# Performance work log

Hardware: AMD Instinct MI355X
Metric: run time of the kernel (lower is better)

The kernel has to match this reference:

```python
import jax, jax.numpy as jnp
import numpy as np

NUM_REL = 5000
NUM_BIN = 32
NUM_EDGES = 200000
DIM = 512
NUM_HEAD = 8
DIM_HID = DIM // NUM_HEAD


def setup_inputs() -> dict:
    key = jax.random.key(0)
    ks = jax.random.split(key, 10)
    emb_rel = jax.random.normal(ks[0], (NUM_REL, DIM), dtype=jnp.float32)
    emb_bin = jax.random.normal(ks[1], (NUM_BIN, DIM), dtype=jnp.float32)
    head = jax.random.randint(ks[2], (NUM_EDGES, 1), 0, NUM_REL)
    tail = jax.random.randint(ks[3], (NUM_EDGES, 1), 0, NUM_REL)
    bins = jax.random.randint(ks[4], (NUM_EDGES, 1), 0, NUM_BIN)
    relation_triplets = jnp.concatenate([head, tail, bins], axis=1).astype(jnp.int64)
    gain = float(np.sqrt(2.0))  # calculate_gain('relu')
    # xavier normal: std = gain * sqrt(2/(fan_in+fan_out))
    std_attn = gain * np.sqrt(2.0 / (3 * DIM + DIM))
    std_aggr = gain * np.sqrt(2.0 / (DIM + DIM))
    std_vec = gain * np.sqrt(2.0 / (NUM_HEAD + DIM_HID))
    W_attn = std_attn * jax.random.normal(ks[5], (DIM, 3 * DIM), dtype=jnp.float32)
    b_attn = jnp.zeros((DIM,), dtype=jnp.float32)
    attn_vec = std_vec * jax.random.normal(ks[6], (1, NUM_HEAD, DIM_HID), dtype=jnp.float32)
    W_aggr = std_aggr * jax.random.normal(ks[7], (DIM, DIM), dtype=jnp.float32)
    b_aggr = jnp.zeros((DIM,), dtype=jnp.float32)
    return {"emb_rel": emb_rel, "emb_bin": emb_bin, "relation_triplets": relation_triplets,
            "W_attn": W_attn, "b_attn": b_attn, "attn_vec": attn_vec,
            "W_aggr": W_aggr, "b_aggr": b_aggr}


def reference(emb_rel, emb_bin, relation_triplets, W_attn, b_attn, attn_vec, W_aggr, b_aggr):
    num_rel = emb_rel.shape[0]
    head = relation_triplets[:, 0]
    tail = relation_triplets[:, 1]
    bins = relation_triplets[:, 2]
    # gather + concat -> [E, 3*D]
    concat = jnp.concatenate([emb_rel[head], emb_bin[bins], emb_rel[tail]], axis=-1)
    h = jax.nn.leaky_relu(concat @ W_attn.T + b_attn, negative_slope=0.2)
    h = h.reshape(-1, NUM_HEAD, DIM_HID)
    attn_raw = jnp.sum(h * attn_vec, axis=-1)  # [E, H]
    # segmented softmax over edges sharing the same head relation
    seg_max = jax.ops.segment_max(attn_raw, head, num_segments=num_rel)  # [R, H]
    seg_max = jnp.where(jnp.isfinite(seg_max), seg_max, 0.0)  # empty segments
    ev = jnp.exp(attn_raw - seg_max[head])  # [E, H]
    seg_sum = jax.ops.segment_sum(ev, head, num_segments=num_rel)  # [R, H]
    beta = ev / (seg_sum[head] + 1e-16)  # [E, H]
    msg = (emb_rel[tail] @ W_aggr.T + b_aggr).reshape(-1, NUM_HEAD, DIM_HID)  # [E, H, Dh]
    out = jax.ops.segment_sum(beta[..., None] * msg, head, num_segments=num_rel)  # [R, H, Dh]
    return out.reshape(num_rel, -1)
```

## Files before the change

kernel.cpp:

```cpp
#include <hip/hip_runtime.h>
#include <hip/hip_bf16.h>

#define NREL 5000
#define NBIN 32
#define NEDGE 200000
#define DIM 512
#define NHEAD 8
#define CAP 256

typedef __attribute__((ext_vector_type(8))) short short8;
typedef __attribute__((ext_vector_type(4))) short short4v;
typedef __attribute__((ext_vector_type(4))) float f32x4;
typedef unsigned short ushort_t;

#define REL_N (NREL * DIM)
#define BIN_N (NBIN * DIM)
#define WATTN_N (DIM * 3 * DIM)
#define WAGGR_N (DIM * DIM)
#define CTOT (REL_N + BIN_N + WATTN_N + WAGGR_N)
#define CONV_BLOCKS (CTOT / 4 / 256)
#define SCAT_BLOCKS ((NEDGE + 255) / 256)

__device__ __forceinline__ float b2f(ushort_t u) {
  unsigned int v = ((unsigned int)u) << 16;
  union { unsigned int i; float f; } c; c.i = v; return c.f;
}
__device__ __forceinline__ ushort_t f2b_rne(float f) {
  union { float f; unsigned int u; } c; c.f = f;
  unsigned int u = c.u;
  return (ushort_t)((u + 0x7FFFu + ((u >> 16) & 1u)) >> 16);
}
__device__ __forceinline__ void gload16(const void* g, void* l) {
  __builtin_amdgcn_global_load_lds(
      (const __attribute__((address_space(1))) void*)g,
      (__attribute__((address_space(3))) void*)l, 16, 0, 0);
}

__global__ void conv_scatter_k(const float* __restrict__ s_rel, const float* __restrict__ s_bin,
                               const float* __restrict__ s_wattn, const float* __restrict__ s_waggr,
                               ushort_t* __restrict__ dst,
                               const int* __restrict__ trip, int* __restrict__ cur,
                               unsigned int* __restrict__ etb) {
  int b = blockIdx.x;
  if (b < CONV_BLOCKS) {
    const int O1 = REL_N, O2 = O1 + BIN_N, O3 = O2 + WATTN_N;
    int i4 = (b * 256 + threadIdx.x) * 4;
    const float* src; int j;
    if (i4 < O1)      { src = s_rel;   j = i4; }
    else if (i4 < O2) { src = s_bin;   j = i4 - O1; }
    else if (i4 < O3) { src = s_wattn; j = i4 - O2; }
    else              { src = s_waggr; j = i4 - O3; }
    float4 v = *(const float4*)(src + j);
    short4v o;
    o[0] = (short)f2b_rne(v.x); o[1] = (short)f2b_rne(v.y);
    o[2] = (short)f2b_rne(v.z); o[3] = (short)f2b_rne(v.w);
    *(short4v*)(dst + i4) = o;
  } else {
    int e = (b - CONV_BLOCKS) * 256 + threadIdx.x;
    if (e >= NEDGE) return;
    int h  = trip[3 * e];
    int ta = trip[3 * e + 1];
    int bi = trip[3 * e + 2];
    h  = min(max(h, 0), NREL - 1);
    ta = min(max(ta, 0), NREL - 1);
    bi = min(max(bi, 0), NBIN - 1);
    int p = atomicAdd(&cur[h], 1);
    if (p < CAP)
      etb[(h << 8) + p] = ((unsigned int)ta << 11) | ((unsigned int)bi << 24);
  }
}

__global__ __launch_bounds__(256) void gemm_k(
    const ushort_t* __restrict__ c_rel, const ushort_t* __restrict__ c_bin,
    const ushort_t* __restrict__ c_wattn, const float* __restrict__ b_attn,
    const ushort_t* __restrict__ c_waggr, const float* __restrict__ b_aggr,
    ushort_t* __restrict__ P1B, ushort_t* __restrict__ PM, ushort_t* __restrict__ P2)
{
  __shared__ ushort_t Alds[64 * 64];
  __shared__ ushort_t Blds[128 * 64];
  int bx = blockIdx.x, by = blockIdx.y;
  const ushort_t* A; int Arows;
  const ushort_t* Bbase; int Bld; int joff;
  const float* bias;
  ushort_t* OUT; int OUTld; int ocolOff;
  int rbase;
  if (bx == 79) {
    if (by >= 4) return;
    A = c_bin; Arows = NBIN; rbase = 0;
    Bbase = c_wattn + 512; Bld = 3 * DIM; joff = 0;
    bias = b_attn;
    OUT = P2; OUTld = DIM; ocolOff = 0;
  } else {
    A = c_rel; Arows = NREL; rbase = bx * 64;
    int seg = by >> 2;
    if (seg == 2)      { Bbase = c_waggr;        Bld = DIM;     bias = b_aggr; }
    else if (seg == 1) { Bbase = c_wattn + 1024; Bld = 3 * DIM; bias = nullptr; }
    else               { Bbase = c_wattn;        Bld = 3 * DIM; bias = nullptr; }
    joff = seg * 512;
    OUT = (seg == 0) ? P1B : PM;
    OUTld = (seg == 0) ? DIM : 1024;
    ocolOff = (seg == 0) ? 0 : 512;
  }
  int tid = threadIdx.x;
  int l = tid & 63, wv = tid >> 6;
  int ctb = by * 128;
  int lr = l >> 3;
  int srcslot = (l & 7) ^ lr;
  const ushort_t* aS0; const ushort_t* aS1;
  const ushort_t* bS0; const ushort_t* bS1; const ushort_t* bS2; const ushort_t* bS3;
  {
    int a0 = wv * 16 + 0 * 8 + lr, a1 = wv * 16 + 1 * 8 + lr;
    aS0 = A + (size_t)min(rbase + a0, Arows - 1) * DIM + srcslot * 8;
    aS1 = A + (size_t)min(rbase + a1, Arows - 1) * DIM + srcslot * 8;
    int c0 = wv * 32 + 0 * 8 + lr, c1 = wv * 32 + 1 * 8 + lr,
        c2 = wv * 32 + 2 * 8 + lr, c3 = wv * 32 + 3 * 8 + lr;
    bS0 = Bbase + (size_t)(ctb + c0 - joff) * Bld + srcslot * 8;
    bS1 = Bbase + (size_t)(ctb + c1 - joff) * Bld + srcslot * 8;
    bS2 = Bbase + (size_t)(ctb + c2 - joff) * Bld + srcslot * 8;
    bS3 = Bbase + (size_t)(ctb + c3 - joff) * Bld + srcslot * 8;
  }
  ushort_t* aD0 = Alds + (wv * 16 + 0) * 64;
  ushort_t* aD1 = Alds + (wv * 16 + 8) * 64;
  ushort_t* bD0 = Blds + (wv * 32 + 0) * 64;
  ushort_t* bD1 = Blds + (wv * 32 + 8) * 64;
  ushort_t* bD2 = Blds + (wv * 32 + 16) * 64;
  ushort_t* bD3 = Blds + (wv * 32 + 24) * 64;

  f32x4 acc[4][2] = {};
  for (int kk = 0; kk < DIM; kk += 64) {
    gload16(aS0 + kk, aD0); gload16(aS1 + kk, aD1);
    gload16(bS0 + kk, bD0); gload16(bS1 + kk, bD1);
    gload16(bS2 + kk, bD2); gload16(bS3 + kk, bD3);
    __syncthreads();
#pragma unroll
    for (int ks = 0; ks < 2; ++ks) {
      int sg = ks * 4 + (l >> 4);
      int sw = (sg ^ (l & 7)) * 8;
      short8 aF[4], bF[2];
#pragma unroll
      for (int m2 = 0; m2 < 4; ++m2) {
        int mrow = m2 * 16 + (l & 15);
        aF[m2] = *(const short8*)(Alds + mrow * 64 + sw);
      }
#pragma unroll
      for (int n = 0; n < 2; ++n) {
        int crow = wv * 32 + n * 16 + (l & 15);
        bF[n] = *(const short8*)(Blds + crow * 64 + sw);
      }
#pragma unroll
      for (int m2 = 0; m2 < 4; ++m2)
#pragma unroll
        for (int n = 0; n < 2; ++n)
          acc[m2][n] = __builtin_amdgcn_mfma_f32_16x16x32_bf16(aF[m2], bF[n], acc[m2][n], 0, 0, 0);
    }
    __syncthreads();
  }
  int r0 = rbase + (l >> 4) * 4;
#pragma unroll
  for (int n = 0; n < 2; ++n) {
    int col = ctb + wv * 32 + n * 16 + (l & 15);
    float bv = bias ? bias[col - joff] : 0.0f;
    int ocol = col - ocolOff;
#pragma unroll
    for (int m2 = 0; m2 < 4; ++m2) {
#pragma unroll
      for (int jj = 0; jj < 4; ++jj) {
        int row = r0 + m2 * 16 + jj;
        if (row < Arows) OUT[(size_t)row * OUTld + ocol] = f2b_rne(acc[m2][n][jj] + bv);
      }
    }
  }
}

#define EDGE_LOAD(TB, P2V, P3V, MV)                                     \
  {                                                                     \
    const char* row_ = PMc + ((TB) & 0x00FFFFFFu);                      \
    P2V = *(const short8*)(p2lds + (((TB) >> 24) << 10) + l16);         \
    P3V = *(const short8*)(row_ + l16);                                 \
    MV  = *(const short8*)(row_ + 1024 + l16);                          \
  }

#define EDGE_COMPUTE(P2V, P3V, MV)                                      \
  {                                                                     \
    float part = 0.0f;                                                  \
    _Pragma("unroll")                                                   \
    for (int j = 0; j < 8; ++j) {                                       \
      float z = p1v[j] + b2f((ushort_t)P2V[j]) + b2f((ushort_t)P3V[j]); \
      part += z * (z > 0.f ? avv[j] : avv02[j]);                        \
    }                                                                   \
    part += __shfl_xor(part, 1);                                        \
    part += __shfl_xor(part, 2);                                        \
    part += __shfl_xor(part, 4);                                        \
    if (part > m + 8.0f) {                                              \
      float f = __expf(m - part);                                       \
      s *= f;                                                           \
      _Pragma("unroll")                                                 \
      for (int j = 0; j < 8; ++j) acc[j] *= f;                          \
      m = part;                                                         \
    }                                                                   \
    float ev = __expf(part - m);                                        \
    s += ev;                                                            \
    _Pragma("unroll")                                                   \
    for (int j = 0; j < 8; ++j) acc[j] += ev * b2f((ushort_t)MV[j]);    \
  }

__global__ __launch_bounds__(256, 6) void aggr2_k(
    const int* __restrict__ cur, const unsigned int* __restrict__ etb,
    const ushort_t* __restrict__ P1B, const ushort_t* __restrict__ PM,
    const ushort_t* __restrict__ P2, const float* __restrict__ avec,
    float* __restrict__ outf)
{
  __shared__ __align__(16) char shmem[32 * DIM * 2];
  __shared__ float ms[4][NHEAD][2];

  int t = threadIdx.x;
  int l = t & 63, wv = t >> 6;
  int p = wv >> 1, sub = wv & 1;
  int r = blockIdx.x * 2 + p;
  int nE = min(cur[r], CAP);
  int base = r << 8;
  int half = nE >> 1;
  int start = sub ? half : 0;
  int cnt = sub ? (nE - half) : half;

  int hd1 = l >> 3;
  int ob = l * 8;
  int l16 = l * 16;

  {
    ushort_t* p2dst = (ushort_t*)shmem;
#pragma unroll
    for (int i = 0; i < 8; ++i) {
      int idx = t * 8 + i * 2048;
      *(short8*)(p2dst + idx) = *(const short8*)(P2 + idx);
    }
  }

  float p1v[8], avv[8], avv02[8];
  {
    short8 p1b = *(const short8*)(P1B + (size_t)r * DIM + ob);
#pragma unroll
    for (int j = 0; j < 8; ++j) {
      p1v[j] = b2f((ushort_t)p1b[j]);
      float a = avec[ob + j];
      avv[j] = a;
      avv02[j] = 0.2f * a;
    }
  }
  float acc[8] = {};
  float m = -INFINITY, s = 0.0f;

  const char* PMc = (const char*)PM;
  const char* p2lds = (const char*)shmem;

  __syncthreads();

  for (int ck = 0; ck < cnt; ck += 64) {
    int ne = min(64, cnt - ck);
    unsigned int tbreg = 0;
    if (l < ne) tbreg = etb[base + start + ck + l];
    short8 p2A, p3A, mvA, p2B, p3B, mvB;
    unsigned int tb0 = (unsigned int)__shfl((int)tbreg, 0);
    EDGE_LOAD(tb0, p2A, p3A, mvA);
    int i = 0;
    while (i + 1 < ne) {
      unsigned int tbb = (unsigned int)__shfl((int)tbreg, i + 1);
      EDGE_LOAD(tbb, p2B, p3B, mvB);
      EDGE_COMPUTE(p2A, p3A, mvA);
      if (i + 2 < ne) {
        unsigned int tba = (unsigned int)__shfl((int)tbreg, i + 2);
        EDGE_LOAD(tba, p2A, p3A, mvA);
      }
      EDGE_COMPUTE(p2B, p3B, mvB);
      i += 2;
    }
    if (i < ne) EDGE_COMPUTE(p2A, p3A, mvA);
  }

  __syncthreads();
  float* red = (float*)shmem;
#pragma unroll
  for (int j = 0; j < 8; ++j) red[wv * DIM + ob + j] = acc[j];
  if ((l & 7) == 0) { ms[wv][hd1][0] = m; ms[wv][hd1][1] = s; }
  __syncthreads();

  int pp = t >> 7;
  int d0 = (t & 127) * 4;
  int h = d0 >> 6;
  int rr = blockIdx.x * 2 + pp;
  float m1 = ms[2 * pp][h][0], s1 = ms[2 * pp][h][1];
  float m2 = ms[2 * pp + 1][h][0], s2 = ms[2 * pp + 1][h][1];
  float M = fmaxf(m1, m2);
  float c1 = (m1 == M) ? 1.0f : __expf(m1 - M);
  float c2 = (m2 == M) ? 1.0f : __expf(m2 - M);
  float S = s1 * c1 + s2 * c2;
  float inv = 1.0f / (S + 1e-16f);
  float4 val;
  val.x = (red[(2 * pp) * DIM + d0]     * c1 + red[(2 * pp + 1) * DIM + d0]     * c2) * inv;
  val.y = (red[(2 * pp) * DIM + d0 + 1] * c1 + red[(2 * pp + 1) * DIM + d0 + 1] * c2) * inv;
  val.z = (red[(2 * pp) * DIM + d0 + 2] * c1 + red[(2 * pp + 1) * DIM + d0 + 2] * c2) * inv;
  val.w = (red[(2 * pp) * DIM + d0 + 3] * c1 + red[(2 * pp + 1) * DIM + d0 + 3] * c2) * inv;
  *(float4*)(outf + (size_t)rr * DIM + d0) = val;
}

extern "C" void kernel_launch(void* const* d_in, const int* in_sizes, int n_in,
                              void* d_out, int out_size, void* d_ws, size_t ws_size,
                              hipStream_t stream) {
  const float* s_rel   = (const float*)d_in[0];
  const float* s_bin   = (const float*)d_in[1];
  const int*   trip    = (const int*)d_in[2];
  const float* s_wattn = (const float*)d_in[3];
  const float* b_attn  = (const float*)d_in[4];
  const float* avec    = (const float*)d_in[5];
  const float* s_waggr = (const float*)d_in[6];
  const float* b_aggr  = (const float*)d_in[7];

  ushort_t* canon = (ushort_t*)d_ws;
  ushort_t* c_rel   = canon;
  ushort_t* c_bin   = c_rel + REL_N;
  ushort_t* c_wattn = c_bin + BIN_N;
  ushort_t* c_waggr = c_wattn + WATTN_N;
  int* cur = (int*)(c_waggr + WAGGR_N);
  unsigned int* etb = (unsigned int*)(cur + NREL);
  ushort_t* P1B = (ushort_t*)(((uintptr_t)(etb + NREL * CAP) + 15) & ~(uintptr_t)15);
  ushort_t* PM  = P1B + (size_t)NREL * DIM;
  ushort_t* P2  = PM + (size_t)NREL * 1024;

  hipMemsetAsync(cur, 0, NREL * sizeof(int), stream);

  conv_scatter_k<<<CONV_BLOCKS + SCAT_BLOCKS, 256, 0, stream>>>(
      s_rel, s_bin, s_wattn, s_waggr, canon, trip, cur, etb);

  dim3 gg(80, 12);
  gemm_k<<<gg, 256, 0, stream>>>(c_rel, c_bin, c_wattn, b_attn, c_waggr, b_aggr,
                                 P1B, PM, P2);

  aggr2_k<<<NREL / 2, 256, 0, stream>>>(cur, etb, P1B, PM, P2, avec, (float*)d_out);
}
```

Baseline: 94.81 us.

## Move edge scatter into GEMM launch and fold counter reset into conversion kernel

Drops the separate memset by zeroing the per-relation counters inside the conversion kernel. The edge bucketing (atomic scatter) moves out of the conversion launch and into 320 extra blocks of the GEMM grid, each handling 625 edges. This removes one launch and lets the scatter overlap with GEMM tiles, but the scatter blocks now compete with GEMM blocks for CUs.

```diff
diff --git a/kernel.cpp b/kernel.cpp
--- a/kernel.cpp
+++ b/kernel.cpp
@@ -19,7 +19,6 @@
 #define WAGGR_N (DIM * DIM)
 #define CTOT (REL_N + BIN_N + WATTN_N + WAGGR_N)
 #define CONV_BLOCKS (CTOT / 4 / 256)
-#define SCAT_BLOCKS ((NEDGE + 255) / 256)
 
 __device__ __forceinline__ float b2f(ushort_t u) {
   unsigned int v = ((unsigned int)u) << 16;
@@ -36,49 +35,54 @@
       (__attribute__((address_space(3))) void*)l, 16, 0, 0);
 }
 
-__global__ void conv_scatter_k(const float* __restrict__ s_rel, const float* __restrict__ s_bin,
-                               const float* __restrict__ s_wattn, const float* __restrict__ s_waggr,
-                               ushort_t* __restrict__ dst,
-                               const int* __restrict__ trip, int* __restrict__ cur,
-                               unsigned int* __restrict__ etb) {
+__global__ void conv_k(const float* __restrict__ s_rel, const float* __restrict__ s_bin,
+                       const float* __restrict__ s_wattn, const float* __restrict__ s_waggr,
+                       ushort_t* __restrict__ dst, int* __restrict__ cur) {
   int b = blockIdx.x;
-  if (b < CONV_BLOCKS) {
-    const int O1 = REL_N, O2 = O1 + BIN_N, O3 = O2 + WATTN_N;
-    int i4 = (b * 256 + threadIdx.x) * 4;
-    const float* src; int j;
-    if (i4 < O1)      { src = s_rel;   j = i4; }
-    else if (i4 < O2) { src = s_bin;   j = i4 - O1; }
-    else if (i4 < O3) { src = s_wattn; j = i4 - O2; }
-    else              { src = s_waggr; j = i4 - O3; }
-    float4 v = *(const float4*)(src + j);
-    short4v o;
-    o[0] = (short)f2b_rne(v.x); o[1] = (short)f2b_rne(v.y);
-    o[2] = (short)f2b_rne(v.z); o[3] = (short)f2b_rne(v.w);
-    *(short4v*)(dst + i4) = o;
-  } else {
-    int e = (b - CONV_BLOCKS) * 256 + threadIdx.x;
-    if (e >= NEDGE) return;
-    int h  = trip[3 * e];
-    int ta = trip[3 * e + 1];
-    int bi = trip[3 * e + 2];
-    h  = min(max(h, 0), NREL - 1);
-    ta = min(max(ta, 0), NREL - 1);
-    bi = min(max(bi, 0), NBIN - 1);
-    int p = atomicAdd(&cur[h], 1);
-    if (p < CAP)
-      etb[(h << 8) + p] = ((unsigned int)ta << 11) | ((unsigned int)bi << 24);
-  }
-}
-
-__global__ __launch_bounds__(256) void gemm_k(
+  if (b < 20) {
+    int i = b * 256 + threadIdx.x;
+    if (i < NREL) cur[i] = 0;
+  }
+  const int O1 = REL_N, O2 = O1 + BIN_N, O3 = O2 + WATTN_N;
+  int i4 = (b * 256 + threadIdx.x) * 4;
+  const float* src; int j;
+  if (i4 < O1)      { src = s_rel;   j = i4; }
+  else if (i4 < O2) { src = s_bin;   j = i4 - O1; }
+  else if (i4 < O3) { src = s_wattn; j = i4 - O2; }
+  else              { src = s_waggr; j = i4 - O3; }
+  float4 v = *(const float4*)(src + j);
+  short4v o;
+  o[0] = (short)f2b_rne(v.x); o[1] = (short)f2b_rne(v.y);
+  o[2] = (short)f2b_rne(v.z); o[3] = (short)f2b_rne(v.w);
+  *(short4v*)(dst + i4) = o;
+}
+
+__global__ __launch_bounds__(256) void gemm_scatter_k(
     const ushort_t* __restrict__ c_rel, const ushort_t* __restrict__ c_bin,
     const ushort_t* __restrict__ c_wattn, const float* __restrict__ b_attn,
     const ushort_t* __restrict__ c_waggr, const float* __restrict__ b_aggr,
-    ushort_t* __restrict__ P1B, ushort_t* __restrict__ PM, ushort_t* __restrict__ P2)
+    ushort_t* __restrict__ P1B, ushort_t* __restrict__ PM, ushort_t* __restrict__ P2,
+    const int* __restrict__ trip, int* __restrict__ cur, unsigned int* __restrict__ etb)
 {
   __shared__ ushort_t Alds[64 * 64];
   __shared__ ushort_t Blds[128 * 64];
   int bx = blockIdx.x, by = blockIdx.y;
+  if (by >= 12) {
+    int sid = (by - 12) * 80 + bx;
+    for (int i = threadIdx.x; i < 625; i += 256) {
+      int e = sid * 625 + i;
+      int h  = trip[3 * e];
+      int ta = trip[3 * e + 1];
+      int bi = trip[3 * e + 2];
+      h  = min(max(h, 0), NREL - 1);
+      ta = min(max(ta, 0), NREL - 1);
+      bi = min(max(bi, 0), NBIN - 1);
+      int p = atomicAdd(&cur[h], 1);
+      if (p < CAP)
+        etb[(h << 8) + p] = ((unsigned int)ta << 11) | ((unsigned int)bi << 24);
+    }
+    return;
+  }
   const ushort_t* A; int Arows;
   const ushort_t* Bbase; int Bld; int joff;
   const float* bias;
@@ -326,14 +330,11 @@
   ushort_t* PM  = P1B + (size_t)NREL * DIM;
   ushort_t* P2  = PM + (size_t)NREL * 1024;
 
-  hipMemsetAsync(cur, 0, NREL * sizeof(int), stream);
-
-  conv_scatter_k<<<CONV_BLOCKS + SCAT_BLOCKS, 256, 0, stream>>>(
-      s_rel, s_bin, s_wattn, s_waggr, canon, trip, cur, etb);
-
-  dim3 gg(80, 12);
-  gemm_k<<<gg, 256, 0, stream>>>(c_rel, c_bin, c_wattn, b_attn, c_waggr, b_aggr,
-                                 P1B, PM, P2);
+  conv_k<<<CONV_BLOCKS, 256, 0, stream>>>(s_rel, s_bin, s_wattn, s_waggr, canon, cur);
+
+  dim3 gg(80, 16);
+  gemm_scatter_k<<<gg, 256, 0, stream>>>(c_rel, c_bin, c_wattn, b_attn, c_waggr, b_aggr,
+                                         P1B, PM, P2, trip, cur, etb);
 
   aggr2_k<<<NREL / 2, 256, 0, stream>>>(cur, etb, P1B, PM, P2, avec, (float*)d_out);
 }
```

Measured after the change: 82.02 us. -13.5%, faster.
